# Kernel tuning notes

Measured on AMD Instinct MI355X. Metric: run time of the kernel, lower is better.

Reference implementation:

```python
import jax, jax.numpy as jnp
import numpy as np

N_HEAD = 16
G_HEADS = 2
D_HEAD = 64
D_MODEL = 1024
HEAD_RATIO = N_HEAD // G_HEADS  # 8
QK_DIM = G_HEADS * D_HEAD       # 128
SCALE = 1.0 / D_HEAD ** 0.5
LN_EPS = 1e-5


def _rel_shift(x):
    # x: [qlen, rlen, B, n] -- Transformer-XL relative shift
    q, r = x.shape[0], x.shape[1]
    x_pad = jnp.pad(x, ((0, 0), (1, 0), (0, 0), (0, 0)))      # [q, r+1, B, n]
    x_pad = x_pad.reshape(r + 1, q, *x.shape[2:])[1:]          # drop first row
    return x_pad.reshape(q, r, *x.shape[2:])


def setup_inputs() -> dict:
    key = jax.random.key(0)
    ks = jax.random.split(key, 9)
    qlen, bsz, levels = 1024, 4, 3
    w = jax.random.normal(ks[0], (qlen, bsz, D_MODEL), jnp.float32)
    r = jax.random.normal(ks[1], (qlen, D_MODEL), jnp.float32)
    r_w_bias = jax.random.normal(ks[2], (G_HEADS, D_HEAD), jnp.float32) * 0.02
    r_r_bias = jax.random.normal(ks[3], (G_HEADS, D_HEAD), jnp.float32) * 0.02
    masks = jax.random.uniform(ks[4], (qlen, qlen, levels), jnp.float32)
    W_qkv = jax.random.normal(ks[5], (2 * QK_DIM + N_HEAD * D_HEAD, D_MODEL), jnp.float32) * 0.02
    W_r = jax.random.normal(ks[6], (QK_DIM, D_MODEL), jnp.float32) * 0.02
    mask_proj = jnp.ones((levels, N_HEAD), jnp.float32)
    W_o = jax.random.normal(ks[7], (D_MODEL, N_HEAD * D_HEAD), jnp.float32) * 0.02
    ln_gamma = jnp.ones((D_MODEL,), jnp.float32)
    ln_beta = jnp.zeros((D_MODEL,), jnp.float32)
    return dict(w=w, r=r, r_w_bias=r_w_bias, r_r_bias=r_r_bias, masks=masks,
                W_qkv=W_qkv, W_r=W_r, mask_proj=mask_proj, W_o=W_o,
                ln_gamma=ln_gamma, ln_beta=ln_beta)


def reference(w, r, r_w_bias, r_r_bias, masks, W_qkv, W_r, mask_proj, W_o, ln_gamma, ln_beta):
    qlen, bsz, _ = w.shape
    rlen = r.shape[0]
    N = qlen  # no mems: klen == qlen == rlen

    w_heads = w @ W_qkv.T                                   # [q, B, 1280]
    r_head_k = (r @ W_r.T).reshape(rlen, G_HEADS, D_HEAD)   # [r, gH, d]
    w_head_q = w_heads[..., :QK_DIM].reshape(qlen, bsz, G_HEADS, D_HEAD)
    w_head_k = w_heads[..., QK_DIM:2 * QK_DIM].reshape(qlen, bsz, G_HEADS, D_HEAD)
    w_head_v = w_heads[..., 2 * QK_DIM:].reshape(qlen, bsz, N_HEAD, D_HEAD)

    AC = jnp.einsum('ibnd,jbnd->ijbn', w_head_q + r_w_bias, w_head_k)
    BD = jnp.einsum('ibnd,jnd->ijbn', w_head_q + r_r_bias, r_head_k)
    BD = _rel_shift(BD)
    attn_score = (AC + BD) * SCALE                           # [N, N, B, gH]

    # per-head mask mixing ('full' projection)
    attn = jnp.transpose(attn_score, (2, 3, 0, 1))           # [B, gH, N, N]
    mw = (masks @ mask_proj).reshape(N, N, G_HEADS, HEAD_RATIO)
    mw = jnp.transpose(mw, (2, 0, 1, 3))                     # [gH, N, N, hr]
    attn = attn[..., None] * mw[None]                        # [B, gH, N, N, hr]
    attn = jnp.transpose(attn, (0, 1, 4, 2, 3)).reshape(bsz, N_HEAD, N, N)
    attn_score = jnp.transpose(attn, (2, 3, 0, 1))           # [N, N, B, H]

    attn_prob = jax.nn.softmax(attn_score, axis=1)
    attn_vec = jnp.einsum('ijbn,jbnd->ibnd', attn_prob, w_head_v)
    attn_vec = attn_vec.reshape(qlen, bsz, N_HEAD * D_HEAD)
    attn_out = attn_vec @ W_o.T                              # [q, B, d_model]

    # post-LN residual
    x = w + attn_out
    mu = jnp.mean(x, axis=-1, keepdims=True)
    var = jnp.mean((x - mu) ** 2, axis=-1, keepdims=True)
    return (x - mu) * jax.lax.rsqrt(var + LN_EPS) * ln_gamma + ln_beta
```

## Files before the change

kernel.cpp:

```cpp
#include <hip/hip_runtime.h>
#include <cstddef>
#include <cstdint>

#define QLEN   1024
#define SCALE  0.125f
#define LN_EPS 1e-5f
#define DMODEL 1024

typedef __bf16 bf16x8 __attribute__((ext_vector_type(8)));
typedef __bf16 bf16x4 __attribute__((ext_vector_type(4)));
typedef float  f32x4  __attribute__((ext_vector_type(4)));

__device__ __forceinline__ void load16_lds(const void* g, void* l) {
  __builtin_amdgcn_global_load_lds(
      (const __attribute__((address_space(1))) unsigned int*)g,
      (__attribute__((address_space(3))) unsigned int*)l, 16, 0, 0);
}

__device__ __forceinline__ void bar_lds() {
  asm volatile("s_waitcnt lgkmcnt(0)" ::: "memory");
  __builtin_amdgcn_s_barrier();
  asm volatile("" ::: "memory");
}

__global__ __launch_bounds__(256) void cast_all(
    const float* __restrict__ w, __bf16* __restrict__ w_bf,
    const float* __restrict__ Wqkv, __bf16* __restrict__ Wqkv_bf,
    const float* __restrict__ r, __bf16* __restrict__ r_bf,
    const float* __restrict__ Wr, __bf16* __restrict__ Wr_bf,
    const float* __restrict__ Wo, __bf16* __restrict__ Wo_bf)
{
  int blk = blockIdx.x;
  const float* in; __bf16* out;
  if (blk < 2048)      { in = w;    out = w_bf;    }
  else if (blk < 2688) { blk -= 2048; in = Wqkv; out = Wqkv_bf; }
  else if (blk < 3200) { blk -= 2688; in = r;    out = r_bf;    }
  else if (blk < 3264) { blk -= 3200; in = Wr;   out = Wr_bf;   }
  else                 { blk -= 3264; in = Wo;   out = Wo_bf;   }
  const size_t i = ((size_t)blk * 256 + threadIdx.x) * 8;
  const float4 a = *(const float4*)&in[i];
  const float4 b = *(const float4*)&in[i + 4];
  bf16x8 o;
  o[0] = (__bf16)a.x; o[1] = (__bf16)a.y; o[2] = (__bf16)a.z; o[3] = (__bf16)a.w;
  o[4] = (__bf16)b.x; o[5] = (__bf16)b.y; o[6] = (__bf16)b.z; o[7] = (__bf16)b.w;
  *(bf16x8*)&out[i] = o;
}

__global__ __launch_bounds__(256) void gemm_proj(
    const __bf16* __restrict__ w_bf, const __bf16* __restrict__ Wqkv_bf,
    const __bf16* __restrict__ r_bf, const __bf16* __restrict__ Wr_bf,
    const float* __restrict__ rwb, const float* __restrict__ rrb,
    __bf16* __restrict__ Qw, __bf16* __restrict__ Qr,
    __bf16* __restrict__ Kb, __bf16* __restrict__ Vt,
    __bf16* __restrict__ Rb)
{
  __shared__ __bf16 Asl[128 * 32];
  __shared__ __bf16 Bsl[64 * 32];
  const int blk = blockIdx.x;
  const bool isR = blk >= 640;
  const __bf16 *A, *B;
  int m0, n0;
  if (!isR) { A = w_bf; B = Wqkv_bf; n0 = (blk % 20) * 64; m0 = (blk / 20) * 128; }
  else      { const int k = blk - 640; A = r_bf; B = Wr_bf;
              n0 = (k % 2) * 64; m0 = (k / 2) * 128; }

  const int tid = threadIdx.x, lane = tid & 63, wv = tid >> 6;
  const int lr = lane & 15, kq = lane >> 4;
  const int srow  = wv * 16 + (lane >> 2);
  const int sslot = lane & 3;
  const int sg0 = (sslot - ((srow >> 1) & 3)) & 3;
  const int sg1 = (sslot - (((srow + 64) >> 1) & 3)) & 3;
  const __bf16* Ag = A + (size_t)(m0 + srow) * 1024;
  const __bf16* Bg = B + (size_t)(n0 + srow) * 1024;
  __bf16* Al = &Asl[srow * 32 + sslot * 8];
  __bf16* Bl = &Bsl[srow * 32 + sslot * 8];

  f32x4 acc[2][4];
#pragma unroll
  for (int mt = 0; mt < 2; ++mt)
#pragma unroll
    for (int nt = 0; nt < 4; ++nt)
      acc[mt][nt] = (f32x4){0.f, 0.f, 0.f, 0.f};

  for (int k0 = 0; k0 < 1024; k0 += 32) {
    load16_lds(Ag + k0 + sg0 * 8, Al);
    load16_lds(Ag + (size_t)64 * 1024 + k0 + sg1 * 8, Al + 64 * 32);
    load16_lds(Bg + k0 + sg0 * 8, Bl);
    __syncthreads();
    bf16x8 af[2], bfr[4];
#pragma unroll
    for (int mt = 0; mt < 2; ++mt) {
      const int row = wv * 32 + mt * 16 + lr;
      af[mt] = *(const bf16x8*)&Asl[row * 32 + ((kq + (row >> 1)) & 3) * 8];
    }
#pragma unroll
    for (int nt = 0; nt < 4; ++nt) {
      const int row = nt * 16 + lr;
      bfr[nt] = *(const bf16x8*)&Bsl[row * 32 + ((kq + (row >> 1)) & 3) * 8];
    }
#pragma unroll
    for (int mt = 0; mt < 2; ++mt)
#pragma unroll
      for (int nt = 0; nt < 4; ++nt)
        acc[mt][nt] = __builtin_amdgcn_mfma_f32_16x16x32_bf16(
            af[mt], bfr[nt], acc[mt][nt], 0, 0, 0);
    __syncthreads();
  }

#pragma unroll
  for (int mt = 0; mt < 2; ++mt) {
    const int row0 = m0 + wv * 32 + mt * 16 + kq * 4;
#pragma unroll
    for (int nt = 0; nt < 4; ++nt) {
      const int gcol = n0 + nt * 16 + lr;
      const f32x4 c = acc[mt][nt];
      if (isR) {
        const int g = gcol >> 6, d = gcol & 63;
#pragma unroll
        for (int reg = 0; reg < 4; ++reg)
          Rb[(size_t)g * 65536 + (size_t)(row0 + reg) * 64 + d] = (__bf16)c[reg];
      } else if (gcol < 128) {
        const int g = gcol >> 6, d = gcol & 63;
        const float bw = rwb[gcol], br = rrb[gcol];
#pragma unroll
        for (int reg = 0; reg < 4; ++reg) {
          const int row = row0 + reg, i = row >> 2, b = row & 3;
          const size_t o = (size_t)(b * 2 + g) * 65536 + (size_t)i * 64 + d;
          Qw[o] = (__bf16)(c[reg] + bw);
          Qr[o] = (__bf16)(c[reg] + br);
        }
      } else if (gcol < 256) {
        const int lc = gcol - 128, g = lc >> 6, d = lc & 63;
#pragma unroll
        for (int reg = 0; reg < 4; ++reg) {
          const int row = row0 + reg, i = row >> 2, b = row & 3;
          Kb[(size_t)(b * 2 + g) * 65536 + (size_t)i * 64 + d] = (__bf16)c[reg];
        }
      } else {
        const int lc = gcol - 256, h = lc >> 6, d = lc & 63;
#pragma unroll
        for (int reg = 0; reg < 4; ++reg) {
          const int row = row0 + reg, i = row >> 2, b = row & 3;
          Vt[((size_t)((b * 16 + h) * 64 + d)) * 1024 + i] = (__bf16)c[reg];
        }
      }
    }
  }
}

__global__ __launch_bounds__(256) void gemm_wo(
    const __bf16* __restrict__ A, const __bf16* __restrict__ B,
    float* __restrict__ C)
{
  __shared__ __bf16 Asl[128 * 32];
  __shared__ __bf16 Bsl[64 * 32];
  const int m0 = blockIdx.y * 128, n0 = blockIdx.x * 64;
  const int tid = threadIdx.x, lane = tid & 63, wv = tid >> 6;
  const int lr = lane & 15, kq = lane >> 4;
  const int srow  = wv * 16 + (lane >> 2);
  const int sslot = lane & 3;
  const int sg0 = (sslot - ((srow >> 1) & 3)) & 3;
  const int sg1 = (sslot - (((srow + 64) >> 1) & 3)) & 3;
  const __bf16* Ag = A + (size_t)(m0 + srow) * 1024;
  const __bf16* Bg = B + (size_t)(n0 + srow) * 1024;
  __bf16* Al = &Asl[srow * 32 + sslot * 8];
  __bf16* Bl = &Bsl[srow * 32 + sslot * 8];

  f32x4 acc[2][4];
#pragma unroll
  for (int mt = 0; mt < 2; ++mt)
#pragma unroll
    for (int nt = 0; nt < 4; ++nt)
      acc[mt][nt] = (f32x4){0.f, 0.f, 0.f, 0.f};

  for (int k0 = 0; k0 < 1024; k0 += 32) {
    load16_lds(Ag + k0 + sg0 * 8, Al);
    load16_lds(Ag + (size_t)64 * 1024 + k0 + sg1 * 8, Al + 64 * 32);
    load16_lds(Bg + k0 + sg0 * 8, Bl);
    __syncthreads();
    bf16x8 af[2], bfr[4];
#pragma unroll
    for (int mt = 0; mt < 2; ++mt) {
      const int row = wv * 32 + mt * 16 + lr;
      af[mt] = *(const bf16x8*)&Asl[row * 32 + ((kq + (row >> 1)) & 3) * 8];
    }
#pragma unroll
    for (int nt = 0; nt < 4; ++nt) {
      const int row = nt * 16 + lr;
      bfr[nt] = *(const bf16x8*)&Bsl[row * 32 + ((kq + (row >> 1)) & 3) * 8];
    }
#pragma unroll
    for (int mt = 0; mt < 2; ++mt)
#pragma unroll
      for (int nt = 0; nt < 4; ++nt)
        acc[mt][nt] = __builtin_amdgcn_mfma_f32_16x16x32_bf16(
            af[mt], bfr[nt], acc[mt][nt], 0, 0, 0);
    __syncthreads();
  }

#pragma unroll
  for (int mt = 0; mt < 2; ++mt) {
    const int row0 = m0 + wv * 32 + mt * 16 + kq * 4;
#pragma unroll
    for (int nt = 0; nt < 4; ++nt) {
      const int col = n0 + nt * 16 + lr;
      const f32x4 c = acc[mt][nt];
#pragma unroll
      for (int reg = 0; reg < 4; ++reg)
        C[(size_t)(row0 + reg) * 1024 + col] = c[reg];
    }
  }
}

__global__ __launch_bounds__(256) void gemm64_bf16(
    const __bf16* __restrict__ Qw, const __bf16* __restrict__ Qr,
    const __bf16* __restrict__ Kb, const __bf16* __restrict__ Rb,
    __bf16* __restrict__ AC, __bf16* __restrict__ BDo)
{
  __shared__ __bf16 Asl[128 * 64];
  __shared__ __bf16 Bsl[128 * 64];
  const int tid = threadIdx.x, lane = tid & 63, wv = tid >> 6;
  const int which = blockIdx.z & 1, bat = blockIdx.z >> 1;
  const int m0 = blockIdx.y * 128, n0 = blockIdx.x * 128;
  const __bf16* Ap = (which ? Qr : Qw) + (size_t)bat * 65536;
  const __bf16* Bp = which ? (Rb + (size_t)(bat & 1) * 65536)
                           : (Kb + (size_t)bat * 65536);
  __bf16* Cp = (which ? BDo : AC) + (size_t)bat * 1048576;

#pragma unroll
  for (int p = 0; p < 4; ++p) {
    const int row = wv * 32 + p * 8 + (lane >> 3);
    const int s = lane & 7;
    const int gc = (s - (row & 7)) & 7;
    load16_lds(Ap + (size_t)(m0 + row) * 64 + gc * 8, &Asl[row * 64 + s * 8]);
    load16_lds(Bp + (size_t)(n0 + row) * 64 + gc * 8, &Bsl[row * 64 + s * 8]);
  }
  __syncthreads();

  const int lr = lane & 15, kq = lane >> 4;
  const int wm = (wv >> 1) * 64, wn = (wv & 1) * 64;
  f32x4 acc[4][4];
#pragma unroll
  for (int mt = 0; mt < 4; ++mt)
#pragma unroll
    for (int nt = 0; nt < 4; ++nt)
      acc[mt][nt] = (f32x4){0.f, 0.f, 0.f, 0.f};

#pragma unroll
  for (int ks = 0; ks < 2; ++ks) {
    const int c = ks * 4 + kq;
    bf16x8 af[4], bfr[4];
#pragma unroll
    for (int mt = 0; mt < 4; ++mt) {
      const int row = wm + mt * 16 + lr;
      af[mt] = *(const bf16x8*)&Asl[row * 64 + ((c + (row & 7)) & 7) * 8];
    }
#pragma unroll
    for (int nt = 0; nt < 4; ++nt) {
      const int row = wn + nt * 16 + lr;
      bfr[nt] = *(const bf16x8*)&Bsl[row * 64 + ((c + (row & 7)) & 7) * 8];
    }
#pragma unroll
    for (int mt = 0; mt < 4; ++mt)
#pragma unroll
      for (int nt = 0; nt < 4; ++nt)
        acc[mt][nt] = __builtin_amdgcn_mfma_f32_16x16x32_bf16(
            af[mt], bfr[nt], acc[mt][nt], 0, 0, 0);
  }

#pragma unroll
  for (int mt = 0; mt < 4; ++mt) {
    const int row0 = m0 + wm + mt * 16 + kq * 4;
#pragma unroll
    for (int nt = 0; nt < 4; ++nt) {
      const int col = n0 + wn + nt * 16 + lr;
      const f32x4 cc = acc[mt][nt];
      if (which) {
#pragma unroll
        for (int reg = 0; reg < 4; ++reg) {
          const int k = row0 + reg;
          const int thr = 1023 - k;
          if (col >= thr) {
            Cp[(size_t)k * 1024 + (col - thr)] = (__bf16)cc[reg];
            if (col == thr && k < 1023)
              Cp[(size_t)k * 1024 + (k + 1)] = (__bf16)0.f;
          } else if (k > 0) {
            Cp[(size_t)(k - 1) * 1024 + (col + k + 1)] = (__bf16)cc[reg];
          }
        }
      } else {
#pragma unroll
        for (int reg = 0; reg < 4; ++reg)
          Cp[(size_t)(row0 + reg) * 1024 + col] = (__bf16)cc[reg];
      }
    }
  }
}

__global__ __launch_bounds__(256) void prep3(
    const __bf16* __restrict__ AC, const __bf16* __restrict__ BDs,
    __bf16* __restrict__ Tg,
    const float* __restrict__ masks, const float* __restrict__ mproj,
    __bf16* __restrict__ Mh)
{
  const int tid = threadIdx.x;
  if (blockIdx.x < 2048) {
    const size_t base = (size_t)blockIdx.x * 4096 + (size_t)tid * 16;
    const bf16x8 a0 = *(const bf16x8*)&AC[base];
    const bf16x8 a1 = *(const bf16x8*)&AC[base + 8];
    const bf16x8 b0 = *(const bf16x8*)&BDs[base];
    const bf16x8 b1 = *(const bf16x8*)&BDs[base + 8];
    bf16x8 o0, o1;
#pragma unroll
    for (int k = 0; k < 8; ++k) {
      o0[k] = (__bf16)(((float)a0[k] + (float)b0[k]) * SCALE);
      o1[k] = (__bf16)(((float)a1[k] + (float)b1[k]) * SCALE);
    }
    *(bf16x8*)&Tg[base] = o0;
    *(bf16x8*)&Tg[base + 8] = o1;
  } else {
    const int blk = blockIdx.x - 2048;
    const size_t ij0 = ((size_t)blk * 256 + tid) * 4;
    const float4 a = *(const float4*)&masks[ij0 * 3];
    const float4 b = *(const float4*)&masks[ij0 * 3 + 4];
    const float4 c = *(const float4*)&masks[ij0 * 3 + 8];
    const float m0[4] = {a.x, a.w, b.z, c.y};
    const float m1[4] = {a.y, b.x, b.w, c.z};
    const float m2[4] = {a.z, b.y, c.x, c.w};
#pragma unroll
    for (int h = 0; h < 16; ++h) {
      const float p0 = mproj[h], p1 = mproj[16 + h], p2 = mproj[32 + h];
      bf16x4 o;
#pragma unroll
      for (int k = 0; k < 4; ++k)
        o[k] = (__bf16)(m0[k] * p0 + m1[k] * p1 + m2[k] * p2);
      *(bf16x4*)&Mh[(size_t)h * 1048576 + ij0] = o;
    }
  }
}

__global__ __launch_bounds__(256, 6) void attn10(
    const __bf16* __restrict__ Tg, const __bf16* __restrict__ Mh,
    const __bf16* __restrict__ Vt, __bf16* __restrict__ av)
{
  __shared__ __bf16 P[2][32 * 128];
  __shared__ float rinvS[32];
  const int tid = threadIdx.x;
  const int i0 = blockIdx.x * 32;
  const int h = blockIdx.y, b = blockIdx.z;
  const int g = h >> 3;
  const size_t bg = (size_t)(b * 2 + g);
  const int r = tid >> 3, li = tid & 7;
  const __bf16* Trow = Tg + bg * 1048576 + (size_t)(i0 + r) * 1024 + li * 8;
  const __bf16* Mrow = Mh + (size_t)h * 1048576 + (size_t)(i0 + r) * 1024 + li * 8;

  const int lane = tid & 63, wv = tid >> 6;
  const int m = lane & 15, kq = lane >> 4;
  const __bf16* vbase = Vt + ((size_t)((b * 16 + h) * 64 + wv * 16 + m)) * 1024 + kq * 8;

  float sum = 0.f;
  f32x4 acc[2][2];
#pragma unroll
  for (int mt = 0; mt < 2; ++mt)
#pragma unroll
    for (int u = 0; u < 2; ++u)
      acc[mt][u] = (f32x4){0.f, 0.f, 0.f, 0.f};

  bf16x8 t[2], mk[2], v[4];
#pragma unroll
  for (int q = 0; q < 2; ++q) {
    t[q]  = *(const bf16x8*)&Trow[q * 64];
    mk[q] = *(const bf16x8*)&Mrow[q * 64];
  }

  for (int ch = 0; ch < 8; ++ch) {
    const int cb = ch & 1;
#pragma unroll
    for (int ks = 0; ks < 4; ++ks)
      v[ks] = *(const bf16x8*)&vbase[(ch * 4 + ks) * 32];
#pragma unroll
    for (int q = 0; q < 2; ++q) {
      bf16x8 p8;
      float s0 = 0.f;
#pragma unroll
      for (int k = 0; k < 8; ++k) {
        const float e = __expf((float)t[q][k] * (float)mk[q][k]);
        s0 += e;
        p8[k] = (__bf16)e;
      }
      sum += s0;
      const int slot = (q * 8 + li) ^ (r & 7);
      *(bf16x8*)&P[cb][r * 128 + slot * 8] = p8;
    }
    if (ch < 7) {
#pragma unroll
      for (int q = 0; q < 2; ++q) {
        t[q]  = *(const bf16x8*)&Trow[(ch + 1) * 128 + q * 64];
        mk[q] = *(const bf16x8*)&Mrow[(ch + 1) * 128 + q * 64];
      }
    }
    bar_lds();
#pragma unroll
    for (int ks = 0; ks < 4; ++ks) {
      const int c = ks * 4 + kq;
#pragma unroll
      for (int mt = 0; mt < 2; ++mt) {
        const int R = mt * 16 + m;
        const bf16x8 a = *(const bf16x8*)&P[cb][R * 128 + ((c ^ (R & 7)) << 3)];
        acc[mt][ks & 1] = __builtin_amdgcn_mfma_f32_16x16x32_bf16(
            a, v[ks], acc[mt][ks & 1], 0, 0, 0);
      }
    }
  }

  sum += __shfl_xor(sum, 1);
  sum += __shfl_xor(sum, 2);
  sum += __shfl_xor(sum, 4);
  if (li == 0) rinvS[r] = 1.f / sum;
  __syncthreads();

#pragma unroll
  for (int mt = 0; mt < 2; ++mt) {
    const f32x4 accf = acc[mt][0] + acc[mt][1];
#pragma unroll
    for (int reg = 0; reg < 4; ++reg) {
      const int row = mt * 16 + kq * 4 + reg;
      av[((size_t)(i0 + row) * 4 + b) * 1024 + h * 64 + wv * 16 + m] =
          (__bf16)(accf[reg] * rinvS[row]);
    }
  }
}

__global__ __launch_bounds__(256) void ln_kernel(
    const float* __restrict__ w, const float* __restrict__ ao,
    const float* __restrict__ gamma, const float* __restrict__ beta,
    float* __restrict__ out)
{
  const int tid = threadIdx.x;
  const int lane = tid & 63, wv = tid >> 6;
  const size_t base = (size_t)blockIdx.x * DMODEL + tid * 4;
  __shared__ float red[8];
  const float4 xw = *(const float4*)&w[base];
  const float4 xa = *(const float4*)&ao[base];
  float x[4] = {xw.x + xa.x, xw.y + xa.y, xw.z + xa.z, xw.w + xa.w};
  float s = (x[0] + x[1]) + (x[2] + x[3]);
  s += __shfl_xor(s, 1);  s += __shfl_xor(s, 2);  s += __shfl_xor(s, 4);
  s += __shfl_xor(s, 8);  s += __shfl_xor(s, 16); s += __shfl_xor(s, 32);
  if (lane == 0) red[wv] = s;
  __syncthreads();
  const float mu = (red[0] + red[1] + red[2] + red[3]) * (1.f / DMODEL);
  float s2 = 0.f;
#pragma unroll
  for (int p = 0; p < 4; ++p) { const float t = x[p] - mu; s2 += t * t; }
  s2 += __shfl_xor(s2, 1);  s2 += __shfl_xor(s2, 2);  s2 += __shfl_xor(s2, 4);
  s2 += __shfl_xor(s2, 8);  s2 += __shfl_xor(s2, 16); s2 += __shfl_xor(s2, 32);
  if (lane == 0) red[4 + wv] = s2;
  __syncthreads();
  const float rs = rsqrtf((red[4] + red[5] + red[6] + red[7]) * (1.f / DMODEL) + LN_EPS);
  const float4 g4 = *(const float4*)&gamma[tid * 4];
  const float4 b4 = *(const float4*)&beta[tid * 4];
  float4 o;
  o.x = (x[0] - mu) * rs * g4.x + b4.x;
  o.y = (x[1] - mu) * rs * g4.y + b4.y;
  o.z = (x[2] - mu) * rs * g4.z + b4.z;
  o.w = (x[3] - mu) * rs * g4.w + b4.w;
  *(float4*)&out[base] = o;
}

extern "C" void kernel_launch(void* const* d_in, const int* in_sizes, int n_in,
                              void* d_out, int out_size, void* d_ws, size_t ws_size,
                              hipStream_t stream)
{
  const float* w     = (const float*)d_in[0];
  const float* r     = (const float*)d_in[1];
  const float* rwb   = (const float*)d_in[2];
  const float* rrb   = (const float*)d_in[3];
  const float* masks = (const float*)d_in[4];
  const float* Wqkv  = (const float*)d_in[5];
  const float* Wr    = (const float*)d_in[6];
  const float* mproj = (const float*)d_in[7];
  const float* Wo    = (const float*)d_in[8];
  const float* gam   = (const float*)d_in[9];
  const float* bet   = (const float*)d_in[10];
  float* out = (float*)d_out;

  float* ws = (float*)d_ws;
  __bf16* w_bf    = (__bf16*)(ws);
  __bf16* Wqkv_bf = (__bf16*)(ws + 2097152);
  __bf16* r_bf    = (__bf16*)(ws + 2752512);
  __bf16* Wr_bf   = (__bf16*)(ws + 3276800);
  __bf16* Qw      = (__bf16*)(ws + 3342336);
  __bf16* Qr      = (__bf16*)(ws + 3604480);
  __bf16* Kb      = (__bf16*)(ws + 3866624);
  __bf16* Rb      = (__bf16*)(ws + 4128768);
  __bf16* Mh      = (__bf16*)(ws);
  __bf16* AC_bf   = (__bf16*)(ws + 8388608);
  float*  ao      = ws + 8388608;
  __bf16* BD_bf   = (__bf16*)(ws + 12582912);
  __bf16* Tg      = (__bf16*)(ws + 16777216);
  __bf16* Vt      = (__bf16*)(ws + 20971520);
  __bf16* av_bf   = (__bf16*)(ws + 23068672);
  __bf16* Wo_bf   = (__bf16*)(ws + 25165824);

  cast_all<<<3776, 256, 0, stream>>>(w, w_bf, Wqkv, Wqkv_bf, r, r_bf,
                                     Wr, Wr_bf, Wo, Wo_bf);
  gemm_proj<<<656, 256, 0, stream>>>(
      w_bf, Wqkv_bf, r_bf, Wr_bf, rwb, rrb, Qw, Qr, Kb, Vt, Rb);
  gemm64_bf16<<<dim3(8, 8, 16), 256, 0, stream>>>(Qw, Qr, Kb, Rb, AC_bf, BD_bf);
  prep3<<<3072, 256, 0, stream>>>(AC_bf, BD_bf, Tg, masks, mproj, Mh);
  attn10<<<dim3(32, 16, 4), 256, 0, stream>>>(Tg, Mh, Vt, av_bf);
  gemm_wo<<<dim3(16, 32), 256, 0, stream>>>(av_bf, Wo_bf, ao);
  ln_kernel<<<4096, 256, 0, stream>>>(w, ao, gam, bet, out);
}
```

Measured before the change: 234.6 us.

## Double-buffer projection GEMMs and fuse AC+BD add into rel-shifted BD GEMM

The projection and output GEMMs now double-buffer their LDS tiles, prefetching the next K slice while MFMAs run on the current one. The combined QK GEMM is split into two kernels: AC is computed first, then the BD kernel reads AC at the rel-shifted destination, adds its own result, scales, and writes the attention-score tensor directly. This removes the BD intermediate buffer and the separate elementwise add pass. The cost is an extra launch, a serial dependency between the two GEMMs, and scattered reads of AC in the BD epilogue.

```diff
diff --git a/kernel.cpp b/kernel.cpp
--- a/kernel.cpp
+++ b/kernel.cpp
@@ -54,8 +54,8 @@
     __bf16* __restrict__ Kb, __bf16* __restrict__ Vt,
     __bf16* __restrict__ Rb)
 {
-  __shared__ __bf16 Asl[128 * 32];
-  __shared__ __bf16 Bsl[64 * 32];
+  __shared__ __bf16 Asl[2][128 * 32];
+  __shared__ __bf16 Bsl[2][64 * 32];
   const int blk = blockIdx.x;
   const bool isR = blk >= 640;
   const __bf16 *A, *B;
@@ -72,8 +72,7 @@
   const int sg1 = (sslot - (((srow + 64) >> 1) & 3)) & 3;
   const __bf16* Ag = A + (size_t)(m0 + srow) * 1024;
   const __bf16* Bg = B + (size_t)(n0 + srow) * 1024;
-  __bf16* Al = &Asl[srow * 32 + sslot * 8];
-  __bf16* Bl = &Bsl[srow * 32 + sslot * 8];
+  const int aoff = srow * 32 + sslot * 8;
 
   f32x4 acc[2][4];
 #pragma unroll
@@ -82,21 +81,32 @@
     for (int nt = 0; nt < 4; ++nt)
       acc[mt][nt] = (f32x4){0.f, 0.f, 0.f, 0.f};
 
+  load16_lds(Ag + sg0 * 8, &Asl[0][aoff]);
+  load16_lds(Ag + (size_t)64 * 1024 + sg1 * 8, &Asl[0][64 * 32 + aoff]);
+  load16_lds(Bg + sg0 * 8, &Bsl[0][aoff]);
+
+  int cb = 0;
   for (int k0 = 0; k0 < 1024; k0 += 32) {
-    load16_lds(Ag + k0 + sg0 * 8, Al);
-    load16_lds(Ag + (size_t)64 * 1024 + k0 + sg1 * 8, Al + 64 * 32);
-    load16_lds(Bg + k0 + sg0 * 8, Bl);
-    __syncthreads();
+    if (k0 + 32 < 1024) {
+      const int nk = k0 + 32, nb = cb ^ 1;
+      load16_lds(Ag + nk + sg0 * 8, &Asl[nb][aoff]);
+      load16_lds(Ag + (size_t)64 * 1024 + nk + sg1 * 8, &Asl[nb][64 * 32 + aoff]);
+      load16_lds(Bg + nk + sg0 * 8, &Bsl[nb][aoff]);
+      asm volatile("s_waitcnt vmcnt(3)" ::: "memory");
+    } else {
+      asm volatile("s_waitcnt vmcnt(0)" ::: "memory");
+    }
+    __builtin_amdgcn_s_barrier();
     bf16x8 af[2], bfr[4];
 #pragma unroll
     for (int mt = 0; mt < 2; ++mt) {
       const int row = wv * 32 + mt * 16 + lr;
-      af[mt] = *(const bf16x8*)&Asl[row * 32 + ((kq + (row >> 1)) & 3) * 8];
+      af[mt] = *(const bf16x8*)&Asl[cb][row * 32 + ((kq + (row >> 1)) & 3) * 8];
     }
 #pragma unroll
     for (int nt = 0; nt < 4; ++nt) {
       const int row = nt * 16 + lr;
-      bfr[nt] = *(const bf16x8*)&Bsl[row * 32 + ((kq + (row >> 1)) & 3) * 8];
+      bfr[nt] = *(const bf16x8*)&Bsl[cb][row * 32 + ((kq + (row >> 1)) & 3) * 8];
     }
 #pragma unroll
     for (int mt = 0; mt < 2; ++mt)
@@ -104,7 +114,8 @@
       for (int nt = 0; nt < 4; ++nt)
         acc[mt][nt] = __builtin_amdgcn_mfma_f32_16x16x32_bf16(
             af[mt], bfr[nt], acc[mt][nt], 0, 0, 0);
-    __syncthreads();
+    bar_lds();
+    cb ^= 1;
   }
 
 #pragma unroll
@@ -152,8 +163,8 @@
     const __bf16* __restrict__ A, const __bf16* __restrict__ B,
     float* __restrict__ C)
 {
-  __shared__ __bf16 Asl[128 * 32];
-  __shared__ __bf16 Bsl[64 * 32];
+  __shared__ __bf16 Asl[2][128 * 32];
+  __shared__ __bf16 Bsl[2][64 * 32];
   const int m0 = blockIdx.y * 128, n0 = blockIdx.x * 64;
   const int tid = threadIdx.x, lane = tid & 63, wv = tid >> 6;
   const int lr = lane & 15, kq = lane >> 4;
@@ -163,8 +174,7 @@
   const int sg1 = (sslot - (((srow + 64) >> 1) & 3)) & 3;
   const __bf16* Ag = A + (size_t)(m0 + srow) * 1024;
   const __bf16* Bg = B + (size_t)(n0 + srow) * 1024;
-  __bf16* Al = &Asl[srow * 32 + sslot * 8];
-  __bf16* Bl = &Bsl[srow * 32 + sslot * 8];
+  const int aoff = srow * 32 + sslot * 8;
 
   f32x4 acc[2][4];
 #pragma unroll
@@ -173,21 +183,32 @@
     for (int nt = 0; nt < 4; ++nt)
       acc[mt][nt] = (f32x4){0.f, 0.f, 0.f, 0.f};
 
+  load16_lds(Ag + sg0 * 8, &Asl[0][aoff]);
+  load16_lds(Ag + (size_t)64 * 1024 + sg1 * 8, &Asl[0][64 * 32 + aoff]);
+  load16_lds(Bg + sg0 * 8, &Bsl[0][aoff]);
+
+  int cb = 0;
   for (int k0 = 0; k0 < 1024; k0 += 32) {
-    load16_lds(Ag + k0 + sg0 * 8, Al);
-    load16_lds(Ag + (size_t)64 * 1024 + k0 + sg1 * 8, Al + 64 * 32);
-    load16_lds(Bg + k0 + sg0 * 8, Bl);
-    __syncthreads();
+    if (k0 + 32 < 1024) {
+      const int nk = k0 + 32, nb = cb ^ 1;
+      load16_lds(Ag + nk + sg0 * 8, &Asl[nb][aoff]);
+      load16_lds(Ag + (size_t)64 * 1024 + nk + sg1 * 8, &Asl[nb][64 * 32 + aoff]);
+      load16_lds(Bg + nk + sg0 * 8, &Bsl[nb][aoff]);
+      asm volatile("s_waitcnt vmcnt(3)" ::: "memory");
+    } else {
+      asm volatile("s_waitcnt vmcnt(0)" ::: "memory");
+    }
+    __builtin_amdgcn_s_barrier();
     bf16x8 af[2], bfr[4];
 #pragma unroll
     for (int mt = 0; mt < 2; ++mt) {
       const int row = wv * 32 + mt * 16 + lr;
-      af[mt] = *(const bf16x8*)&Asl[row * 32 + ((kq + (row >> 1)) & 3) * 8];
+      af[mt] = *(const bf16x8*)&Asl[cb][row * 32 + ((kq + (row >> 1)) & 3) * 8];
     }
 #pragma unroll
     for (int nt = 0; nt < 4; ++nt) {
       const int row = nt * 16 + lr;
-      bfr[nt] = *(const bf16x8*)&Bsl[row * 32 + ((kq + (row >> 1)) & 3) * 8];
+      bfr[nt] = *(const bf16x8*)&Bsl[cb][row * 32 + ((kq + (row >> 1)) & 3) * 8];
     }
 #pragma unroll
     for (int mt = 0; mt < 2; ++mt)
@@ -195,7 +216,8 @@
       for (int nt = 0; nt < 4; ++nt)
         acc[mt][nt] = __builtin_amdgcn_mfma_f32_16x16x32_bf16(
             af[mt], bfr[nt], acc[mt][nt], 0, 0, 0);
-    __syncthreads();
+    bar_lds();
+    cb ^= 1;
   }
 
 #pragma unroll
@@ -212,20 +234,18 @@
   }
 }
 
-__global__ __launch_bounds__(256) void gemm64_bf16(
-    const __bf16* __restrict__ Qw, const __bf16* __restrict__ Qr,
-    const __bf16* __restrict__ Kb, const __bf16* __restrict__ Rb,
-    __bf16* __restrict__ AC, __bf16* __restrict__ BDo)
+__global__ __launch_bounds__(256) void gemm64_AC(
+    const __bf16* __restrict__ Qw, const __bf16* __restrict__ Kb,
+    __bf16* __restrict__ AC)
 {
   __shared__ __bf16 Asl[128 * 64];
   __shared__ __bf16 Bsl[128 * 64];
   const int tid = threadIdx.x, lane = tid & 63, wv = tid >> 6;
-  const int which = blockIdx.z & 1, bat = blockIdx.z >> 1;
+  const int bat = blockIdx.z;
   const int m0 = blockIdx.y * 128, n0 = blockIdx.x * 128;
-  const __bf16* Ap = (which ? Qr : Qw) + (size_t)bat * 65536;
-  const __bf16* Bp = which ? (Rb + (size_t)(bat & 1) * 65536)
-                           : (Kb + (size_t)bat * 65536);
-  __bf16* Cp = (which ? BDo : AC) + (size_t)bat * 1048576;
+  const __bf16* Ap = Qw + (size_t)bat * 65536;
+  const __bf16* Bp = Kb + (size_t)bat * 65536;
+  __bf16* Cp = AC + (size_t)bat * 1048576;
 
 #pragma unroll
   for (int p = 0; p < 4; ++p) {
@@ -275,67 +295,114 @@
     for (int nt = 0; nt < 4; ++nt) {
       const int col = n0 + wn + nt * 16 + lr;
       const f32x4 cc = acc[mt][nt];
-      if (which) {
-#pragma unroll
-        for (int reg = 0; reg < 4; ++reg) {
-          const int k = row0 + reg;
-          const int thr = 1023 - k;
-          if (col >= thr) {
-            Cp[(size_t)k * 1024 + (col - thr)] = (__bf16)cc[reg];
-            if (col == thr && k < 1023)
-              Cp[(size_t)k * 1024 + (k + 1)] = (__bf16)0.f;
-          } else if (k > 0) {
-            Cp[(size_t)(k - 1) * 1024 + (col + k + 1)] = (__bf16)cc[reg];
+#pragma unroll
+      for (int reg = 0; reg < 4; ++reg)
+        Cp[(size_t)(row0 + reg) * 1024 + col] = (__bf16)cc[reg];
+    }
+  }
+}
+
+__global__ __launch_bounds__(256) void gemm64_BDT(
+    const __bf16* __restrict__ Qr, const __bf16* __restrict__ Rb,
+    const __bf16* __restrict__ AC, __bf16* __restrict__ Tg)
+{
+  __shared__ __bf16 Asl[128 * 64];
+  __shared__ __bf16 Bsl[128 * 64];
+  const int tid = threadIdx.x, lane = tid & 63, wv = tid >> 6;
+  const int bat = blockIdx.z;
+  const int m0 = blockIdx.y * 128, n0 = blockIdx.x * 128;
+  const __bf16* Ap = Qr + (size_t)bat * 65536;
+  const __bf16* Bp = Rb + (size_t)(bat & 1) * 65536;
+  const __bf16* ACb = AC + (size_t)bat * 1048576;
+  __bf16* Tb = Tg + (size_t)bat * 1048576;
+
+#pragma unroll
+  for (int p = 0; p < 4; ++p) {
+    const int row = wv * 32 + p * 8 + (lane >> 3);
+    const int s = lane & 7;
+    const int gc = (s - (row & 7)) & 7;
+    load16_lds(Ap + (size_t)(m0 + row) * 64 + gc * 8, &Asl[row * 64 + s * 8]);
+    load16_lds(Bp + (size_t)(n0 + row) * 64 + gc * 8, &Bsl[row * 64 + s * 8]);
+  }
+  __syncthreads();
+
+  const int lr = lane & 15, kq = lane >> 4;
+  const int wm = (wv >> 1) * 64, wn = (wv & 1) * 64;
+  f32x4 acc[4][4];
+#pragma unroll
+  for (int mt = 0; mt < 4; ++mt)
+#pragma unroll
+    for (int nt = 0; nt < 4; ++nt)
+      acc[mt][nt] = (f32x4){0.f, 0.f, 0.f, 0.f};
+
+#pragma unroll
+  for (int ks = 0; ks < 2; ++ks) {
+    const int c = ks * 4 + kq;
+    bf16x8 af[4], bfr[4];
+#pragma unroll
+    for (int mt = 0; mt < 4; ++mt) {
+      const int row = wm + mt * 16 + lr;
+      af[mt] = *(const bf16x8*)&Asl[row * 64 + ((c + (row & 7)) & 7) * 8];
+    }
+#pragma unroll
+    for (int nt = 0; nt < 4; ++nt) {
+      const int row = wn + nt * 16 + lr;
+      bfr[nt] = *(const bf16x8*)&Bsl[row * 64 + ((c + (row & 7)) & 7) * 8];
+    }
+#pragma unroll
+    for (int mt = 0; mt < 4; ++mt)
+#pragma unroll
+      for (int nt = 0; nt < 4; ++nt)
+        acc[mt][nt] = __builtin_amdgcn_mfma_f32_16x16x32_bf16(
+            af[mt], bfr[nt], acc[mt][nt], 0, 0, 0);
+  }
+
+#pragma unroll
+  for (int mt = 0; mt < 4; ++mt) {
+    const int row0 = m0 + wm + mt * 16 + kq * 4;
+#pragma unroll
+    for (int nt = 0; nt < 4; ++nt) {
+      const int col = n0 + wn + nt * 16 + lr;
+      const f32x4 cc = acc[mt][nt];
+#pragma unroll
+      for (int reg = 0; reg < 4; ++reg) {
+        const int k = row0 + reg;
+        const int thr = 1023 - k;
+        if (col >= thr) {
+          const size_t dst = (size_t)k * 1024 + (col - thr);
+          Tb[dst] = (__bf16)(((float)ACb[dst] + cc[reg]) * SCALE);
+          if (col == thr && k < 1023) {
+            const size_t d2 = (size_t)k * 1024 + (k + 1);
+            Tb[d2] = (__bf16)((float)ACb[d2] * SCALE);
           }
+        } else if (k > 0) {
+          const size_t dst = (size_t)(k - 1) * 1024 + (col + k + 1);
+          Tb[dst] = (__bf16)(((float)ACb[dst] + cc[reg]) * SCALE);
         }
-      } else {
-#pragma unroll
-        for (int reg = 0; reg < 4; ++reg)
-          Cp[(size_t)(row0 + reg) * 1024 + col] = (__bf16)cc[reg];
       }
     }
   }
 }
 
-__global__ __launch_bounds__(256) void prep3(
-    const __bf16* __restrict__ AC, const __bf16* __restrict__ BDs,
-    __bf16* __restrict__ Tg,
+__global__ __launch_bounds__(256) void prep_mask(
     const float* __restrict__ masks, const float* __restrict__ mproj,
     __bf16* __restrict__ Mh)
 {
-  const int tid = threadIdx.x;
-  if (blockIdx.x < 2048) {
-    const size_t base = (size_t)blockIdx.x * 4096 + (size_t)tid * 16;
-    const bf16x8 a0 = *(const bf16x8*)&AC[base];
-    const bf16x8 a1 = *(const bf16x8*)&AC[base + 8];
-    const bf16x8 b0 = *(const bf16x8*)&BDs[base];
-    const bf16x8 b1 = *(const bf16x8*)&BDs[base + 8];
-    bf16x8 o0, o1;
-#pragma unroll
-    for (int k = 0; k < 8; ++k) {
-      o0[k] = (__bf16)(((float)a0[k] + (float)b0[k]) * SCALE);
-      o1[k] = (__bf16)(((float)a1[k] + (float)b1[k]) * SCALE);
-    }
-    *(bf16x8*)&Tg[base] = o0;
-    *(bf16x8*)&Tg[base + 8] = o1;
-  } else {
-    const int blk = blockIdx.x - 2048;
-    const size_t ij0 = ((size_t)blk * 256 + tid) * 4;
-    const float4 a = *(const float4*)&masks[ij0 * 3];
-    const float4 b = *(const float4*)&masks[ij0 * 3 + 4];
-    const float4 c = *(const float4*)&masks[ij0 * 3 + 8];
-    const float m0[4] = {a.x, a.w, b.z, c.y};
-    const float m1[4] = {a.y, b.x, b.w, c.z};
-    const float m2[4] = {a.z, b.y, c.x, c.w};
-#pragma unroll
-    for (int h = 0; h < 16; ++h) {
-      const float p0 = mproj[h], p1 = mproj[16 + h], p2 = mproj[32 + h];
-      bf16x4 o;
-#pragma unroll
-      for (int k = 0; k < 4; ++k)
-        o[k] = (__bf16)(m0[k] * p0 + m1[k] * p1 + m2[k] * p2);
-      *(bf16x4*)&Mh[(size_t)h * 1048576 + ij0] = o;
-    }
+  const size_t ij0 = ((size_t)blockIdx.x * 256 + threadIdx.x) * 4;
+  const float4 a = *(const float4*)&masks[ij0 * 3];
+  const float4 b = *(const float4*)&masks[ij0 * 3 + 4];
+  const float4 c = *(const float4*)&masks[ij0 * 3 + 8];
+  const float m0[4] = {a.x, a.w, b.z, c.y};
+  const float m1[4] = {a.y, b.x, b.w, c.z};
+  const float m2[4] = {a.z, b.y, c.x, c.w};
+#pragma unroll
+  for (int h = 0; h < 16; ++h) {
+    const float p0 = mproj[h], p1 = mproj[16 + h], p2 = mproj[32 + h];
+    bf16x4 o;
+#pragma unroll
+    for (int k = 0; k < 4; ++k)
+      o[k] = (__bf16)(m0[k] * p0 + m1[k] * p1 + m2[k] * p2);
+    *(bf16x4*)&Mh[(size_t)h * 1048576 + ij0] = o;
   }
 }
 
@@ -496,7 +563,6 @@
   __bf16* Mh      = (__bf16*)(ws);
   __bf16* AC_bf   = (__bf16*)(ws + 8388608);
   float*  ao      = ws + 8388608;
-  __bf16* BD_bf   = (__bf16*)(ws + 12582912);
   __bf16* Tg      = (__bf16*)(ws + 16777216);
   __bf16* Vt      = (__bf16*)(ws + 20971520);
   __bf16* av_bf   = (__bf16*)(ws + 23068672);
@@ -506,8 +572,9 @@
                                      Wr, Wr_bf, Wo, Wo_bf);
   gemm_proj<<<656, 256, 0, stream>>>(
       w_bf, Wqkv_bf, r_bf, Wr_bf, rwb, rrb, Qw, Qr, Kb, Vt, Rb);
-  gemm64_bf16<<<dim3(8, 8, 16), 256, 0, stream>>>(Qw, Qr, Kb, Rb, AC_bf, BD_bf);
-  prep3<<<3072, 256, 0, stream>>>(AC_bf, BD_bf, Tg, masks, mproj, Mh);
+  gemm64_AC<<<dim3(8, 8, 8), 256, 0, stream>>>(Qw, Kb, AC_bf);
+  gemm64_BDT<<<dim3(8, 8, 8), 256, 0, stream>>>(Qr, Rb, AC_bf, Tg);
+  prep_mask<<<1024, 256, 0, stream>>>(masks, mproj, Mh);
   attn10<<<dim3(32, 16, 4), 256, 0, stream>>>(Tg, Mh, Vt, av_bf);
   gemm_wo<<<dim3(16, 32), 256, 0, stream>>>(av_bf, Wo_bf, ao);
   ln_kernel<<<4096, 256, 0, stream>>>(w, ao, gam, bet, out);
```

Measured after the change: 251.0 us. 1.07x slower.
